# Optimization experiments

Hardware: AMD Instinct MI355X
Metric: run time of the kernel (lower is better)

Reference implementation:

```python
import jax, jax.numpy as jnp
import numpy as np

DIM = 256
HEADS = 8
WS = 7          # window_size
WN = 8          # window_num per side
H = W = WS * WN # 56
B = 32
MLP_HIDDEN = 4 * DIM
SCALE = (DIM // HEADS) ** -0.5
LN_EPS = 1e-5


def _rel_index(ws):
    # pairwise relative position index inside a ws x ws window (dense 0..(2ws-1)^2-1,
    # so remap_position_index is the identity relabeling)
    ch, cw = np.meshgrid(np.arange(ws), np.arange(ws), indexing='ij')
    cf = np.stack([ch.ravel(), cw.ravel()])            # (2, ws*ws)
    rel = cf[:, :, None] - cf[:, None, :]              # (2, N, N)
    rel = rel.transpose(1, 2, 0).astype(np.int32)
    rel[..., 0] += ws - 1
    rel[..., 1] += ws - 1
    rel[..., 0] *= 2 * ws - 1
    return rel.sum(-1)                                 # (N, N) in [0, (2ws-1)^2)


def _layernorm(x, g, b):
    m = x.mean(-1, keepdims=True)
    v = ((x - m) ** 2).mean(-1, keepdims=True)
    return (x - m) * jax.lax.rsqrt(v + LN_EPS) * g + b


def _mhsa(x, qkv_w, qkv_b, proj_w, proj_b, bias):
    # x: (B_, N, C); bias: (nH, N, N) or None
    B_, N, C = x.shape
    hd = C // HEADS
    qkv = (x @ qkv_w.T + qkv_b).reshape(B_, N, 3, HEADS, hd).transpose(2, 0, 3, 1, 4)
    q, k, v = qkv[0], qkv[1], qkv[2]
    attn = jnp.einsum('bhqd,bhkd->bhqk', q * SCALE, k)
    if bias is not None:
        attn = attn + bias[None]
    attn = jax.nn.softmax(attn, axis=-1)
    out = jnp.einsum('bhqk,bhkd->bhqd', attn, v).transpose(0, 2, 1, 3).reshape(B_, N, C)
    return out @ proj_w.T + proj_b


def setup_inputs() -> dict:
    key = jax.random.key(0)
    ks = jax.random.split(key, 8)
    f32 = jnp.float32
    return {
        'regional_tokens': jax.random.normal(ks[0], (B, WN * WN, DIM), f32),
        'x': jax.random.normal(ks[1], (B, H * W, DIM), f32),
        'norm1_g': jnp.ones((DIM,), f32), 'norm1_b': jnp.zeros((DIM,), f32),
        'norm2_g': jnp.ones((DIM,), f32), 'norm2_b': jnp.zeros((DIM,), f32),
        'norm3_g': jnp.ones((DIM,), f32), 'norm3_b': jnp.zeros((DIM,), f32),
        'qkv_w': jax.random.normal(ks[2], (3 * DIM, DIM), f32) * 0.02,
        'qkv_b': jnp.zeros((3 * DIM,), f32),
        'proj_w': jax.random.normal(ks[3], (DIM, DIM), f32) * 0.02,
        'proj_b': jnp.zeros((DIM,), f32),
        'bias_table': jax.random.normal(ks[4], ((2 * WS - 1) ** 2, HEADS), f32) * 0.02,
        'fc1_w': jax.random.normal(ks[5], (MLP_HIDDEN, DIM), f32) * 0.02,
        'fc1_b': jnp.zeros((MLP_HIDDEN,), f32),
        'fc2_w': jax.random.normal(ks[6], (DIM, MLP_HIDDEN), f32) * 0.02,
        'fc2_b': jnp.zeros((DIM,), f32),
        'rel_index': jnp.asarray(_rel_index(WS)),
    }


def reference(regional_tokens, x, norm1_g, norm1_b, norm2_g, norm2_b, norm3_g, norm3_b,
              qkv_w, qkv_b, proj_w, proj_b, bias_table, fc1_w, fc1_b, fc2_w, fc2_b,
              rel_index):
    Bb, L, C = x.shape
    nW = regional_tokens.shape[1]
    ws2 = WS * WS
    # --- RSA: attention over regional tokens (no relative bias) ---
    regional_tokens = regional_tokens + _mhsa(
        _layernorm(regional_tokens, norm1_g, norm1_b), qkv_w, qkv_b, proj_w, proj_b, None)
    # --- window partition of x: (B,H,W,C) -> (nW*B, ws*ws, C) (batch-major) ---
    xw = x.reshape(Bb, H // WS, WS, W // WS, WS, C)
    xw = xw.transpose(0, 1, 3, 2, 4, 5).reshape(-1, ws2, C)
    # regional tokens reshaped window-major, exactly as the torch code does
    reg = regional_tokens.transpose(1, 0, 2).reshape(nW * Bb, 1, C)
    t = jnp.concatenate([reg, xw], axis=1)  # (nW*B, 1+ws2, C)
    # --- LSA relative position bias, zero-padded for the regional token ---
    bias = bias_table[rel_index]                       # (ws2, ws2, nH)
    bias = jnp.pad(bias, ((1, 0), (1, 0), (0, 0)))      # (1+ws2, 1+ws2, nH)
    bias = bias.transpose(2, 0, 1)                      # (nH, N, N)
    t = t + _mhsa(_layernorm(t, norm2_g, norm2_b), qkv_w, qkv_b, proj_w, proj_b, bias)
    # --- MLP ---
    h = _layernorm(t, norm3_g, norm3_b)
    h = jax.nn.gelu(h @ fc1_w.T + fc1_b, approximate=False) @ fc2_w.T + fc2_b
    t = t + h
    # --- split back ---
    reg_out = t[:, 0, :].reshape(nW, Bb, C).transpose(1, 0, 2)   # (B, nW, C)
    xw = t[:, 1:, :].reshape(Bb, H // WS, W // WS, WS, WS, C)
    x_out = xw.transpose(0, 1, 3, 2, 4, 5).reshape(Bb, L, C)
    return reg_out, x_out
```

## Files before the change

kernel.cpp:

```cpp
#include <hip/hip_runtime.h>
#include <math.h>

#define SCALE_Q 0.17677669529663687f

typedef __attribute__((ext_vector_type(8))) short bf16x8;
typedef __attribute__((ext_vector_type(4))) float f32x4;
typedef __attribute__((ext_vector_type(4))) unsigned short u16x4;

static __device__ __forceinline__ unsigned short f2bf(float f) {
    unsigned int u = __float_as_uint(f);
    u += 0x7FFF + ((u >> 16) & 1);
    return (unsigned short)(u >> 16);
}

static __device__ __forceinline__ float gelu_fast(float v) {
    float s = v * (0.7978845608f + 0.0356774081f * v * v);
    float e = __expf(-2.0f * s);
    return v * __builtin_amdgcn_rcpf(1.0f + e);
}

__global__ void prep_kernel(const float* __restrict__ qkv_w, const float* __restrict__ proj_w,
                            const float* __restrict__ fc1_w, const float* __restrict__ fc2_w,
                            const float* __restrict__ bias_table, const int* __restrict__ rel_index,
                            unsigned short* __restrict__ wq, unsigned short* __restrict__ wp,
                            unsigned short* __restrict__ w1, unsigned short* __restrict__ w2,
                            float* __restrict__ bias_pad) {
    int tid = blockIdx.x * blockDim.x + threadIdx.x;
    int stride = gridDim.x * blockDim.x;
    for (int i = tid; i < 768 * 256; i += stride) wq[i] = f2bf(qkv_w[i]);
    for (int i = tid; i < 256 * 256; i += stride) wp[i] = f2bf(proj_w[i]);
    for (int i = tid; i < 1024 * 256; i += stride) w1[i] = f2bf(fc1_w[i]);
    for (int i = tid; i < 256 * 1024; i += stride) w2[i] = f2bf(fc2_w[i]);
    for (int i = tid; i < 8 * 64 * 64; i += stride) {
        int h = i >> 12, q = (i >> 6) & 63, k = i & 63;
        float v;
        if (k >= 50) v = -1e30f;
        else if (q == 0 || k == 0 || q >= 50) v = 0.f;
        else v = bias_table[rel_index[(q - 1) * 49 + (k - 1)] * 8 + h];
        bias_pad[i] = v;
    }
}

template <int IS_RSA>
__global__ __launch_bounds__(1024, 4) void attn_kernel(
    const float* __restrict__ reg_tok, const float* __restrict__ x,
    const float* __restrict__ reg2_in, float* __restrict__ out,
    const float* __restrict__ ln_g, const float* __restrict__ ln_b,
    const unsigned short* __restrict__ wq, const float* __restrict__ qkv_b,
    const unsigned short* __restrict__ wp, const float* __restrict__ proj_b,
    const float* __restrict__ bias_pad) {
    __shared__ __align__(16) unsigned char smem[140288];
    unsigned short* regA = (unsigned short*)smem;
    unsigned short* regB = (unsigned short*)(smem + 36864);
    unsigned short* vT   = (unsigned short*)(smem + 103424);

    const int tid = threadIdx.x;
    const int lane = tid & 63;
    const int wid = tid >> 6;
    const int l15 = lane & 15;
    const int lg = lane >> 4;
    const int u = blockIdx.x;
    const int NV = IS_RSA ? 64 : 50;
    const f32x4 fzero = {0.f, 0.f, 0.f, 0.f};

    int reg_off = 0, xb = 0, wi = 0, wj = 0;
    if (!IS_RSA) {
        reg_off = ((u & 31) * 64 + (u >> 5)) * 256;
        xb = u >> 6;
        int xn = u & 63;
        wi = xn >> 3; wj = xn & 7;
    }

    for (int r = wid; r < 64; r += 16) {
        if (r < NV) {
            const float* src;
            if (IS_RSA) src = reg_tok + (u * 64 + r) * 256;
            else if (r == 0) src = reg2_in + reg_off;
            else {
                int p = r - 1;
                src = x + (xb * 3136 + (wi * 7 + p / 7) * 56 + (wj * 7 + p % 7)) * 256;
            }
            f32x4 v = *(const f32x4*)(src + lane * 4);
            float s = v[0] + v[1] + v[2] + v[3];
            float s2 = v[0] * v[0] + v[1] * v[1] + v[2] * v[2] + v[3] * v[3];
            #pragma unroll
            for (int m = 1; m < 64; m <<= 1) { s += __shfl_xor(s, m); s2 += __shfl_xor(s2, m); }
            float mean = s * 0.00390625f;
            float rstd = rsqrtf(s2 * 0.00390625f - mean * mean + 1e-5f);
            u16x4 o;
            #pragma unroll
            for (int j = 0; j < 4; ++j) {
                int c = lane * 4 + j;
                o[j] = f2bf((v[j] - mean) * rstd * ln_g[c] + ln_b[c]);
            }
            *(u16x4*)(regA + r * 264 + lane * 4) = o;
        } else {
            u16x4 z = {0, 0, 0, 0};
            *(u16x4*)(regA + r * 264 + lane * 4) = z;
        }
    }
    __syncthreads();

    const int h = wid >> 1;
    const int qb = (wid & 1) * 32;

    {
        f32x4 acc[4][3];
        #pragma unroll
        for (int mi = 0; mi < 4; ++mi)
            #pragma unroll
            for (int t = 0; t < 3; ++t) acc[mi][t] = fzero;
        #pragma unroll
        for (int ks = 0; ks < 8; ++ks) {
            int k = ks * 32 + lg * 8;
            bf16x8 a[4], b[3];
            #pragma unroll
            for (int mi = 0; mi < 4; ++mi) a[mi] = *(const bf16x8*)(regA + (mi * 16 + l15) * 264 + k);
            #pragma unroll
            for (int t = 0; t < 3; ++t) b[t] = *(const bf16x8*)(wq + (wid * 48 + t * 16 + l15) * 256 + k);
            #pragma unroll
            for (int mi = 0; mi < 4; ++mi)
                #pragma unroll
                for (int t = 0; t < 3; ++t)
                    acc[mi][t] = __builtin_amdgcn_mfma_f32_16x16x32_bf16(a[mi], b[t], acc[mi][t], 0, 0, 0);
        }
        #pragma unroll
        for (int mi = 0; mi < 4; ++mi)
            #pragma unroll
            for (int t = 0; t < 3; ++t) {
                int col = wid * 48 + t * 16 + l15;
                float bias = qkv_b[col];
                #pragma unroll
                for (int r = 0; r < 4; ++r) {
                    int row = mi * 16 + lg * 4 + r;
                    unsigned short hv = f2bf(acc[mi][t][r] + bias);
                    if (col < 512) regB[row * 520 + col] = hv;
                    else vT[(col - 512) * 72 + row] = hv;
                }
            }
    }

    f32x4 bv[4][2];
    if (!IS_RSA) {
        #pragma unroll
        for (int mi = 0; mi < 4; ++mi)
            #pragma unroll
            for (int nj = 0; nj < 2; ++nj)
                bv[mi][nj] = *(const f32x4*)(bias_pad + h * 4096 + (qb + nj * 16 + l15) * 64 + mi * 16 + lg * 4);
    }
    __syncthreads();

    f32x4 st[4][2];
    {
        int k0 = h * 32 + lg * 8;
        bf16x8 af[4], bfq[2];
        #pragma unroll
        for (int mi = 0; mi < 4; ++mi) af[mi] = *(const bf16x8*)(regB + (mi * 16 + l15) * 520 + 256 + k0);
        #pragma unroll
        for (int nj = 0; nj < 2; ++nj) bfq[nj] = *(const bf16x8*)(regB + (qb + nj * 16 + l15) * 520 + k0);
        #pragma unroll
        for (int mi = 0; mi < 4; ++mi)
            #pragma unroll
            for (int nj = 0; nj < 2; ++nj)
                st[mi][nj] = __builtin_amdgcn_mfma_f32_16x16x32_bf16(af[mi], bfq[nj], fzero, 0, 0, 0);
    }

    u16x4 pf[4][2];
    #pragma unroll
    for (int nj = 0; nj < 2; ++nj) {
        float ps[4][4];
        float mx = -3.0e38f;
        #pragma unroll
        for (int mi = 0; mi < 4; ++mi)
            #pragma unroll
            for (int r = 0; r < 4; ++r) {
                float t = st[mi][nj][r] * SCALE_Q;
                if (!IS_RSA) t += bv[mi][nj][r];
                ps[mi][r] = t;
                mx = fmaxf(mx, t);
            }
        mx = fmaxf(mx, __shfl_xor(mx, 16));
        mx = fmaxf(mx, __shfl_xor(mx, 32));
        float sum = 0.f;
        #pragma unroll
        for (int mi = 0; mi < 4; ++mi)
            #pragma unroll
            for (int r = 0; r < 4; ++r) { ps[mi][r] = __expf(ps[mi][r] - mx); sum += ps[mi][r]; }
        sum += __shfl_xor(sum, 16);
        sum += __shfl_xor(sum, 32);
        float inv = __builtin_amdgcn_rcpf(sum);
        #pragma unroll
        for (int mi = 0; mi < 4; ++mi) {
            u16x4 p4;
            #pragma unroll
            for (int r = 0; r < 4; ++r) p4[r] = f2bf(ps[mi][r] * inv);
            pf[mi][nj] = p4;
        }
    }

    f32x4 ov[2][2];
    #pragma unroll
    for (int m2 = 0; m2 < 2; ++m2) { ov[m2][0] = fzero; ov[m2][1] = fzero; }
    #pragma unroll
    for (int kt = 0; kt < 4; ++kt) {
        bf16x8 pb[2];
        #pragma unroll
        for (int nj = 0; nj < 2; ++nj) {
            bf16x8 t;
            t[0] = (short)pf[kt][nj][0]; t[1] = (short)pf[kt][nj][1];
            t[2] = (short)pf[kt][nj][2]; t[3] = (short)pf[kt][nj][3];
            t[4] = 0; t[5] = 0; t[6] = 0; t[7] = 0;
            pb[nj] = t;
        }
        #pragma unroll
        for (int m2 = 0; m2 < 2; ++m2) {
            u16x4 av = *(const u16x4*)(vT + (h * 32 + m2 * 16 + l15) * 72 + kt * 16 + lg * 4);
            bf16x8 a8;
            a8[0] = (short)av[0]; a8[1] = (short)av[1]; a8[2] = (short)av[2]; a8[3] = (short)av[3];
            a8[4] = 0; a8[5] = 0; a8[6] = 0; a8[7] = 0;
            #pragma unroll
            for (int nj = 0; nj < 2; ++nj)
                ov[m2][nj] = __builtin_amdgcn_mfma_f32_16x16x32_bf16(a8, pb[nj], ov[m2][nj], 0, 0, 0);
        }
    }
    #pragma unroll
    for (int m2 = 0; m2 < 2; ++m2)
        #pragma unroll
        for (int nj = 0; nj < 2; ++nj) {
            u16x4 o4;
            #pragma unroll
            for (int r = 0; r < 4; ++r) o4[r] = f2bf(ov[m2][nj][r]);
            *(u16x4*)(regA + (qb + nj * 16 + l15) * 264 + h * 32 + m2 * 16 + lg * 4) = o4;
        }
    __syncthreads();

    {
        int nb = wid * 16;
        f32x4 acc[4];
        #pragma unroll
        for (int mi = 0; mi < 4; ++mi) acc[mi] = fzero;
        #pragma unroll
        for (int ks = 0; ks < 8; ++ks) {
            int k = ks * 32 + lg * 8;
            bf16x8 a[4], b;
            #pragma unroll
            for (int mi = 0; mi < 4; ++mi) a[mi] = *(const bf16x8*)(regA + (mi * 16 + l15) * 264 + k);
            b = *(const bf16x8*)(wp + (nb + l15) * 256 + k);
            #pragma unroll
            for (int mi = 0; mi < 4; ++mi)
                acc[mi] = __builtin_amdgcn_mfma_f32_16x16x32_bf16(a[mi], b, acc[mi], 0, 0, 0);
        }
        int col = nb + l15;
        float pb = proj_b[col];
        #pragma unroll
        for (int mi = 0; mi < 4; ++mi)
            #pragma unroll
            for (int r = 0; r < 4; ++r) {
                int row = mi * 16 + lg * 4 + r;
                if (row < NV) {
                    float val = acc[mi][r] + pb;
                    if (IS_RSA) {
                        int off = (u * 64 + row) * 256 + col;
                        out[off] = val + reg_tok[off];
                    } else if (row == 0) {
                        out[reg_off + col] = val + reg2_in[reg_off + col];
                    } else {
                        int p = row - 1;
                        int off = (xb * 3136 + (wi * 7 + p / 7) * 56 + (wj * 7 + p % 7)) * 256 + col;
                        out[524288 + off] = val + x[off];
                    }
                }
            }
    }
}

__global__ __launch_bounds__(512, 4) void mlp_kernel(
    float* __restrict__ dout,
    const float* __restrict__ ln_g, const float* __restrict__ ln_b,
    const unsigned short* __restrict__ w1, const float* __restrict__ b1,
    const unsigned short* __restrict__ w2, const float* __restrict__ b2) {
    __shared__ __align__(16) unsigned short xln[64 * 264];
    __shared__ __align__(16) unsigned short hld[64 * 264];
    const int tid = threadIdx.x;
    const int lane = tid & 63;
    const int wid = tid >> 6;
    const int l15 = lane & 15;
    const int lg = lane >> 4;
    const int u = blockIdx.x;
    const f32x4 fzero = {0.f, 0.f, 0.f, 0.f};

    int reg_off = ((u & 31) * 64 + (u >> 5)) * 256;
    int xb = u >> 6;
    int xn = u & 63;
    int wi = xn >> 3, wj = xn & 7;
    float* xsec = dout + 524288;

    for (int r = wid; r < 64; r += 8) {
        if (r < 50) {
            const float* src = (r == 0)
                ? (dout + reg_off)
                : (xsec + (xb * 3136 + (wi * 7 + (r - 1) / 7) * 56 + (wj * 7 + (r - 1) % 7)) * 256);
            f32x4 v = *(const f32x4*)(src + lane * 4);
            float s = v[0] + v[1] + v[2] + v[3];
            float s2 = v[0] * v[0] + v[1] * v[1] + v[2] * v[2] + v[3] * v[3];
            #pragma unroll
            for (int m = 1; m < 64; m <<= 1) { s += __shfl_xor(s, m); s2 += __shfl_xor(s2, m); }
            float mean = s * 0.00390625f;
            float rstd = rsqrtf(s2 * 0.00390625f - mean * mean + 1e-5f);
            u16x4 o;
            #pragma unroll
            for (int j = 0; j < 4; ++j) {
                int c = lane * 4 + j;
                o[j] = f2bf((v[j] - mean) * rstd * ln_g[c] + ln_b[c]);
            }
            *(u16x4*)(xln + r * 264 + lane * 4) = o;
        } else {
            u16x4 z = {0, 0, 0, 0};
            *(u16x4*)(xln + r * 264 + lane * 4) = z;
        }
    }
    __syncthreads();

    f32x4 acc2[4][2];
    #pragma unroll
    for (int mi = 0; mi < 4; ++mi) { acc2[mi][0] = fzero; acc2[mi][1] = fzero; }

    for (int c = 0; c < 4; ++c) {
        f32x4 acc1[4][2];
        #pragma unroll
        for (int mi = 0; mi < 4; ++mi) { acc1[mi][0] = fzero; acc1[mi][1] = fzero; }
        int hb = c * 256 + wid * 32;
        #pragma unroll
        for (int ks = 0; ks < 8; ++ks) {
            int k = ks * 32 + lg * 8;
            bf16x8 a[4], b[2];
            #pragma unroll
            for (int mi = 0; mi < 4; ++mi) a[mi] = *(const bf16x8*)(xln + (mi * 16 + l15) * 264 + k);
            #pragma unroll
            for (int ni = 0; ni < 2; ++ni) b[ni] = *(const bf16x8*)(w1 + (hb + ni * 16 + l15) * 256 + k);
            #pragma unroll
            for (int mi = 0; mi < 4; ++mi)
                #pragma unroll
                for (int ni = 0; ni < 2; ++ni)
                    acc1[mi][ni] = __builtin_amdgcn_mfma_f32_16x16x32_bf16(a[mi], b[ni], acc1[mi][ni], 0, 0, 0);
        }
        #pragma unroll
        for (int mi = 0; mi < 4; ++mi)
            #pragma unroll
            for (int ni = 0; ni < 2; ++ni) {
                int hc = wid * 32 + ni * 16 + l15;
                float bb = b1[c * 256 + hc];
                #pragma unroll
                for (int r = 0; r < 4; ++r) {
                    int row = mi * 16 + lg * 4 + r;
                    float v = acc1[mi][ni][r] + bb;
                    hld[row * 264 + hc] = f2bf(gelu_fast(v));
                }
            }
        __syncthreads();
        #pragma unroll
        for (int ks = 0; ks < 8; ++ks) {
            int k = ks * 32 + lg * 8;
            bf16x8 a[4], b[2];
            #pragma unroll
            for (int mi = 0; mi < 4; ++mi) a[mi] = *(const bf16x8*)(hld + (mi * 16 + l15) * 264 + k);
            #pragma unroll
            for (int ni = 0; ni < 2; ++ni)
                b[ni] = *(const bf16x8*)(w2 + (wid * 32 + ni * 16 + l15) * 1024 + c * 256 + k);
            #pragma unroll
            for (int mi = 0; mi < 4; ++mi)
                #pragma unroll
                for (int ni = 0; ni < 2; ++ni)
                    acc2[mi][ni] = __builtin_amdgcn_mfma_f32_16x16x32_bf16(a[mi], b[ni], acc2[mi][ni], 0, 0, 0);
        }
        __syncthreads();
    }
    #pragma unroll
    for (int mi = 0; mi < 4; ++mi)
        #pragma unroll
        for (int ni = 0; ni < 2; ++ni) {
            int col = wid * 32 + ni * 16 + l15;
            float bb = b2[col];
            #pragma unroll
            for (int r = 0; r < 4; ++r) {
                int row = mi * 16 + lg * 4 + r;
                if (row < 50) {
                    float* dst = (row == 0)
                        ? (dout + reg_off + col)
                        : (xsec + (xb * 3136 + (wi * 7 + (row - 1) / 7) * 56 + (wj * 7 + (row - 1) % 7)) * 256 + col);
                    *dst = acc2[mi][ni][r] + bb + *dst;
                }
            }
        }
}

extern "C" void kernel_launch(void* const* d_in, const int* in_sizes, int n_in,
                              void* d_out, int out_size, void* d_ws, size_t ws_size,
                              hipStream_t stream) {
    const float* regional = (const float*)d_in[0];
    const float* x = (const float*)d_in[1];
    const float* n1g = (const float*)d_in[2];
    const float* n1b = (const float*)d_in[3];
    const float* n2g = (const float*)d_in[4];
    const float* n2b = (const float*)d_in[5];
    const float* n3g = (const float*)d_in[6];
    const float* n3b = (const float*)d_in[7];
    const float* qkvw = (const float*)d_in[8];
    const float* qkvb = (const float*)d_in[9];
    const float* projw = (const float*)d_in[10];
    const float* projb = (const float*)d_in[11];
    const float* btab = (const float*)d_in[12];
    const float* f1w = (const float*)d_in[13];
    const float* f1b = (const float*)d_in[14];
    const float* f2w = (const float*)d_in[15];
    const float* f2b = (const float*)d_in[16];
    const int* relidx = (const int*)d_in[17];

    unsigned char* ws = (unsigned char*)d_ws;
    unsigned short* wq = (unsigned short*)(ws);
    unsigned short* wp = (unsigned short*)(ws + 393216);
    unsigned short* w1 = (unsigned short*)(ws + 524288);
    unsigned short* w2 = (unsigned short*)(ws + 1048576);
    float* bias_pad    = (float*)(ws + 1572864);
    float* reg2        = (float*)(ws + 1703936);

    float* out = (float*)d_out;

    prep_kernel<<<512, 256, 0, stream>>>(qkvw, projw, f1w, f2w, btab, relidx, wq, wp, w1, w2, bias_pad);
    attn_kernel<1><<<32, 1024, 0, stream>>>(regional, x, nullptr, reg2, n1g, n1b, wq, qkvb, wp, projb, nullptr);
    attn_kernel<0><<<2048, 1024, 0, stream>>>(regional, x, reg2, out, n2g, n2b, wq, qkvb, wp, projb, bias_pad);
    mlp_kernel<<<2048, 512, 0, stream>>>(out, n3g, n3b, w1, f1b, w2, f2b);
}
```

Measured before the change: 541.8 us.

## Process MLP over flat contiguous token rows in 128-row tiles

The MLP kernel no longer works per 50-token window padded to 64 rows. It treats the output as a flat array of independent token rows and processes 128 contiguous rows per 1024-thread block, so each weight fragment is reused across more real rows. This removes the padded-row compute and the scattered window-to-image address math in the load and store. The cost is double the LDS per block and a grid of 800 blocks, which may leave an uneven tail across CUs.

```diff
diff --git a/kernel.cpp b/kernel.cpp
--- a/kernel.cpp
+++ b/kernel.cpp
@@ -274,52 +274,43 @@
     }
 }
 
-__global__ __launch_bounds__(512, 4) void mlp_kernel(
+__global__ __launch_bounds__(1024, 4) void mlp_kernel(
     float* __restrict__ dout,
     const float* __restrict__ ln_g, const float* __restrict__ ln_b,
     const unsigned short* __restrict__ w1, const float* __restrict__ b1,
     const unsigned short* __restrict__ w2, const float* __restrict__ b2) {
-    __shared__ __align__(16) unsigned short xln[64 * 264];
-    __shared__ __align__(16) unsigned short hld[64 * 264];
+    __shared__ __align__(16) unsigned short xln[128 * 264];
+    __shared__ __align__(16) unsigned short hld[128 * 264];
     const int tid = threadIdx.x;
     const int lane = tid & 63;
     const int wid = tid >> 6;
     const int l15 = lane & 15;
     const int lg = lane >> 4;
-    const int u = blockIdx.x;
+    const int row0 = blockIdx.x * 128;
     const f32x4 fzero = {0.f, 0.f, 0.f, 0.f};
 
-    int reg_off = ((u & 31) * 64 + (u >> 5)) * 256;
-    int xb = u >> 6;
-    int xn = u & 63;
-    int wi = xn >> 3, wj = xn & 7;
-    float* xsec = dout + 524288;
-
-    for (int r = wid; r < 64; r += 8) {
-        if (r < 50) {
-            const float* src = (r == 0)
-                ? (dout + reg_off)
-                : (xsec + (xb * 3136 + (wi * 7 + (r - 1) / 7) * 56 + (wj * 7 + (r - 1) % 7)) * 256);
-            f32x4 v = *(const f32x4*)(src + lane * 4);
-            float s = v[0] + v[1] + v[2] + v[3];
-            float s2 = v[0] * v[0] + v[1] * v[1] + v[2] * v[2] + v[3] * v[3];
-            #pragma unroll
-            for (int m = 1; m < 64; m <<= 1) { s += __shfl_xor(s, m); s2 += __shfl_xor(s2, m); }
-            float mean = s * 0.00390625f;
-            float rstd = rsqrtf(s2 * 0.00390625f - mean * mean + 1e-5f);
-            u16x4 o;
-            #pragma unroll
-            for (int j = 0; j < 4; ++j) {
-                int c = lane * 4 + j;
-                o[j] = f2bf((v[j] - mean) * rstd * ln_g[c] + ln_b[c]);
-            }
-            *(u16x4*)(xln + r * 264 + lane * 4) = o;
-        } else {
-            u16x4 z = {0, 0, 0, 0};
-            *(u16x4*)(xln + r * 264 + lane * 4) = z;
-        }
+    #pragma unroll
+    for (int i = 0; i < 8; ++i) {
+        int r = wid * 8 + i;
+        f32x4 v = *(const f32x4*)(dout + (row0 + r) * 256 + lane * 4);
+        float s = v[0] + v[1] + v[2] + v[3];
+        float s2 = v[0] * v[0] + v[1] * v[1] + v[2] * v[2] + v[3] * v[3];
+        #pragma unroll
+        for (int m = 1; m < 64; m <<= 1) { s += __shfl_xor(s, m); s2 += __shfl_xor(s2, m); }
+        float mean = s * 0.00390625f;
+        float rstd = rsqrtf(s2 * 0.00390625f - mean * mean + 1e-5f);
+        u16x4 o;
+        #pragma unroll
+        for (int j = 0; j < 4; ++j) {
+            int c = lane * 4 + j;
+            o[j] = f2bf((v[j] - mean) * rstd * ln_g[c] + ln_b[c]);
+        }
+        *(u16x4*)(xln + r * 264 + lane * 4) = o;
     }
     __syncthreads();
+
+    const int wm = wid >> 3;
+    const int wn = wid & 7;
 
     f32x4 acc2[4][2];
     #pragma unroll
@@ -329,15 +320,16 @@
         f32x4 acc1[4][2];
         #pragma unroll
         for (int mi = 0; mi < 4; ++mi) { acc1[mi][0] = fzero; acc1[mi][1] = fzero; }
-        int hb = c * 256 + wid * 32;
         #pragma unroll
         for (int ks = 0; ks < 8; ++ks) {
             int k = ks * 32 + lg * 8;
             bf16x8 a[4], b[2];
             #pragma unroll
-            for (int mi = 0; mi < 4; ++mi) a[mi] = *(const bf16x8*)(xln + (mi * 16 + l15) * 264 + k);
-            #pragma unroll
-            for (int ni = 0; ni < 2; ++ni) b[ni] = *(const bf16x8*)(w1 + (hb + ni * 16 + l15) * 256 + k);
+            for (int mi = 0; mi < 4; ++mi)
+                a[mi] = *(const bf16x8*)(xln + (wm * 64 + mi * 16 + l15) * 264 + k);
+            #pragma unroll
+            for (int ni = 0; ni < 2; ++ni)
+                b[ni] = *(const bf16x8*)(w1 + (c * 256 + wn * 32 + ni * 16 + l15) * 256 + k);
             #pragma unroll
             for (int mi = 0; mi < 4; ++mi)
                 #pragma unroll
@@ -348,11 +340,11 @@
         for (int mi = 0; mi < 4; ++mi)
             #pragma unroll
             for (int ni = 0; ni < 2; ++ni) {
-                int hc = wid * 32 + ni * 16 + l15;
+                int hc = wn * 32 + ni * 16 + l15;
                 float bb = b1[c * 256 + hc];
                 #pragma unroll
                 for (int r = 0; r < 4; ++r) {
-                    int row = mi * 16 + lg * 4 + r;
+                    int row = wm * 64 + mi * 16 + lg * 4 + r;
                     float v = acc1[mi][ni][r] + bb;
                     hld[row * 264 + hc] = f2bf(gelu_fast(v));
                 }
@@ -363,10 +355,11 @@
             int k = ks * 32 + lg * 8;
             bf16x8 a[4], b[2];
             #pragma unroll
-            for (int mi = 0; mi < 4; ++mi) a[mi] = *(const bf16x8*)(hld + (mi * 16 + l15) * 264 + k);
+            for (int mi = 0; mi < 4; ++mi)
+                a[mi] = *(const bf16x8*)(hld + (wm * 64 + mi * 16 + l15) * 264 + k);
             #pragma unroll
             for (int ni = 0; ni < 2; ++ni)
-                b[ni] = *(const bf16x8*)(w2 + (wid * 32 + ni * 16 + l15) * 1024 + c * 256 + k);
+                b[ni] = *(const bf16x8*)(w2 + (wn * 32 + ni * 16 + l15) * 1024 + c * 256 + k);
             #pragma unroll
             for (int mi = 0; mi < 4; ++mi)
                 #pragma unroll
@@ -379,17 +372,13 @@
     for (int mi = 0; mi < 4; ++mi)
         #pragma unroll
         for (int ni = 0; ni < 2; ++ni) {
-            int col = wid * 32 + ni * 16 + l15;
+            int col = wn * 32 + ni * 16 + l15;
             float bb = b2[col];
             #pragma unroll
             for (int r = 0; r < 4; ++r) {
-                int row = mi * 16 + lg * 4 + r;
-                if (row < 50) {
-                    float* dst = (row == 0)
-                        ? (dout + reg_off + col)
-                        : (xsec + (xb * 3136 + (wi * 7 + (row - 1) / 7) * 56 + (wj * 7 + (row - 1) % 7)) * 256 + col);
-                    *dst = acc2[mi][ni][r] + bb + *dst;
-                }
+                int row = row0 + wm * 64 + mi * 16 + lg * 4 + r;
+                float* dst = dout + row * 256 + col;
+                *dst = acc2[mi][ni][r] + bb + *dst;
             }
         }
 }
@@ -429,5 +418,5 @@
     prep_kernel<<<512, 256, 0, stream>>>(qkvw, projw, f1w, f2w, btab, relidx, wq, wp, w1, w2, bias_pad);
     attn_kernel<1><<<32, 1024, 0, stream>>>(regional, x, nullptr, reg2, n1g, n1b, wq, qkvb, wp, projb, nullptr);
     attn_kernel<0><<<2048, 1024, 0, stream>>>(regional, x, reg2, out, n2g, n2b, wq, qkvb, wp, projb, bias_pad);
-    mlp_kernel<<<2048, 512, 0, stream>>>(out, n3g, n3b, w1, f1b, w2, f2b);
-}
+    mlp_kernel<<<800, 1024, 0, stream>>>(out, n3g, n3b, w1, f1b, w2, f2b);
+}
```

Measured after the change: 567.9 us. +4.8%, slower.
